# Kernel optimization log

Measured on AMD Instinct MI355X. Metric: run time of the kernel, lower is better.

The kernel has to match this reference:

```python
import jax, jax.numpy as jnp
import numpy as np
import math

B, T, E, H = 2, 2048, 1024, 16
D = E // H  # head_dim = 64


def setup_inputs() -> dict:
    key = jax.random.key(0)
    ks = jax.random.split(key, 8)
    s = 1.0 / math.sqrt(E)
    x = jax.random.normal(ks[0], (B, T, E), dtype=jnp.float32)
    # Linear weights stored as [in, out] so y = x @ W (equivalent to torch x @ W.T)
    Wq = jax.random.normal(ks[1], (E, E), dtype=jnp.float32) * s
    Wk = jax.random.normal(ks[2], (E, E), dtype=jnp.float32) * s
    Wv = jax.random.normal(ks[3], (E, E), dtype=jnp.float32) * s
    Wa = jax.random.normal(ks[4], (E, H), dtype=jnp.float32) * s
    Wg = jax.random.normal(ks[5], (E, E), dtype=jnp.float32) * s
    Wo = jax.random.normal(ks[6], (E, E), dtype=jnp.float32) * s
    A_log = jnp.linspace(0.0, math.log(16.0), H, dtype=jnp.float32)
    dt_bias = jnp.zeros((H,), dtype=jnp.float32)
    rms_w = jnp.ones((D,), dtype=jnp.float32)
    return {"x": x, "Wq": Wq, "Wk": Wk, "Wv": Wv, "Wa": Wa, "Wg": Wg,
            "Wo": Wo, "A_log": A_log, "dt_bias": dt_bias, "rms_w": rms_w}


def _l2norm(t):
    n = jnp.linalg.norm(t, axis=-1, keepdims=True)
    return t / jnp.maximum(n, 1e-12)


def reference(x, Wq, Wk, Wv, Wa, Wg, Wo, A_log, dt_bias, rms_w):
    b, seq_len, e = x.shape
    h = A_log.shape[0]
    d = e // h
    # QKV projections, L2-normalize q and k over head_dim -> [b, h, t, d]
    q = _l2norm((x @ Wq).reshape(b, seq_len, h, d)).transpose(0, 2, 1, 3)
    k = _l2norm((x @ Wk).reshape(b, seq_len, h, d)).transpose(0, 2, 1, 3)
    v = (x @ Wv).reshape(b, seq_len, h, d).transpose(0, 2, 1, 3)
    # scalar decay alpha in (0,1]: exp(-exp(A_log) * softplus(x @ Wa + dt_bias))
    dt = jax.nn.softplus(x @ Wa + dt_bias)           # [b, t, h]
    alpha = jnp.exp(-jnp.exp(A_log) * dt)            # [b, t, h]
    # decay mask L_ij = prod_{s=j+1}^{i} alpha_s (i >= j), via cumulative log-sum
    cum_log = jnp.cumsum(jnp.log(alpha + 1e-8), axis=1).transpose(0, 2, 1)  # [b, h, t]
    log_l = cum_log[..., :, None] - cum_log[..., None, :]                   # [b, h, t, t]
    causal = jnp.tril(jnp.ones((seq_len, seq_len), dtype=bool))
    l_mat = jnp.where(causal, jnp.exp(log_l), 0.0)
    # quadratic form: Y = (L * Q K^T) V
    scores = jnp.einsum('bhid,bhjd->bhij', q, k) * l_mat
    out = jnp.einsum('bhij,bhjd->bhid', scores, v)   # [b, h, t, d]
    # RMSNorm over head_dim (eps=1e-6)
    out = out * jax.lax.rsqrt(jnp.mean(out * out, axis=-1, keepdims=True) + 1e-6) * rms_w
    out = out.transpose(0, 2, 1, 3).reshape(b, seq_len, e)
    gate = jax.nn.silu(x @ Wg)
    return (out * gate) @ Wo
```

## Files before the change

kernel.cpp:

```cpp
#include <hip/hip_runtime.h>
#include <hip/hip_bf16.h>
#include <math.h>

#define B_ 2
#define T_ 2048
#define E_ 1024
#define H_ 16
#define D_ 64
#define MTOK (B_*T_)

typedef __bf16 bf16;
typedef __bf16 bf16x8 __attribute__((ext_vector_type(8)));
typedef __bf16 bf16x4 __attribute__((ext_vector_type(4)));
typedef float  f32x4  __attribute__((ext_vector_type(4)));

__device__ __forceinline__ void gl_lds16(const void* g, void* l) {
    __builtin_amdgcn_global_load_lds(
        (const __attribute__((address_space(1))) void*)g,
        (__attribute__((address_space(3))) void*)l, 16, 0, 0);
}

__global__ __launch_bounds__(256) void prep_weights_kernel(
    const float* __restrict__ Wq, const float* __restrict__ Wk,
    const float* __restrict__ Wv, const float* __restrict__ Wg,
    const float* __restrict__ Wo, const float* __restrict__ Wa,
    bf16* __restrict__ WTqh, bf16* __restrict__ WTql,
    bf16* __restrict__ WTvg, bf16* __restrict__ WTo,
    float* __restrict__ WaT) {
    const int tid = threadIdx.x;
    if (blockIdx.x >= 1280) {
        int idx = (blockIdx.x - 1280) * 256 + tid;
        WaT[idx] = Wa[(idx & 1023)*H_ + (idx >> 10)];
        return;
    }
    __shared__ float ts[64][65];
    const int seg = blockIdx.x >> 8;
    const int bid = blockIdx.x & 255;
    const float* src = (seg == 0) ? Wq : (seg == 1) ? Wk : (seg == 2) ? Wv
                     : (seg == 3) ? Wg : Wo;
    const int bx = bid & 15, by = bid >> 4;
    {
        const int r = tid >> 2, cb = (tid & 3) * 16;
        const float* s = src + (size_t)(by*64 + r)*1024 + bx*64 + cb;
#pragma unroll
        for (int j = 0; j < 4; ++j) {
            float4 v = *(const float4*)(s + j*4);
            ts[r][cb + j*4 + 0] = v.x; ts[r][cb + j*4 + 1] = v.y;
            ts[r][cb + j*4 + 2] = v.z; ts[r][cb + j*4 + 3] = v.w;
        }
    }
    __syncthreads();
    const int c = tid >> 2, rb = (tid & 3) * 16;
    const size_t obase = (size_t)(bx*64 + c)*1024 + by*64 + rb;
    if (seg < 2) {
        bf16* dh = ((seg == 0) ? WTqh : WTqh + (size_t)1024*1024);
        bf16* dl = ((seg == 0) ? WTql : WTql + (size_t)1024*1024);
#pragma unroll
        for (int half = 0; half < 2; ++half) {
            bf16x8 hv, lv;
#pragma unroll
            for (int e = 0; e < 8; ++e) {
                float v = ts[rb + half*8 + e][c];
                bf16 h = (bf16)v;
                hv[e] = h;
                lv[e] = (bf16)(v - (float)h);
            }
            *(bf16x8*)(dh + obase + half*8) = hv;
            *(bf16x8*)(dl + obase + half*8) = lv;
        }
    } else {
        bf16* dst = (seg == 2) ? WTvg : (seg == 3) ? (WTvg + (size_t)1024*1024) : WTo;
#pragma unroll
        for (int half = 0; half < 2; ++half) {
            bf16x8 hv;
#pragma unroll
            for (int e = 0; e < 8; ++e)
                hv[e] = (bf16)ts[rb + half*8 + e][c];
            *(bf16x8*)(dst + obase + half*8) = hv;
        }
    }
}

__global__ __launch_bounds__(256) void dtx_kernel(const float* __restrict__ x,
                                                  const float* __restrict__ WaT,
                                                  const float* __restrict__ A_log,
                                                  const float* __restrict__ dt_bias,
                                                  float* __restrict__ lg,
                                                  bf16* __restrict__ xh,
                                                  bf16* __restrict__ xl) {
    __shared__ float xs[16][1032];
    const int tb = blockIdx.x * 16;
    const int tid = threadIdx.x;
#pragma unroll
    for (int v = tid; v < 2048; v += 256) {
        int row = v >> 7, c8 = (v & 127) * 8;
        const float* src = x + (size_t)(tb + row)*E_ + c8;
        float4 a = *(const float4*)src;
        float4 b = *(const float4*)(src + 4);
        float va[8] = {a.x, a.y, a.z, a.w, b.x, b.y, b.z, b.w};
        bf16x8 hv, lv;
#pragma unroll
        for (int j = 0; j < 8; ++j) {
            xs[row][c8+j] = va[j];
            bf16 h = (bf16)va[j];
            hv[j] = h;
            lv[j] = (bf16)(va[j] - (float)h);
        }
        *(bf16x8*)(xh + (size_t)(tb + row)*E_ + c8) = hv;
        *(bf16x8*)(xl + (size_t)(tb + row)*E_ + c8) = lv;
    }
    __syncthreads();
    const int i = tid >> 4, h = tid & 15;
    const float* wrow = WaT + (size_t)h*1024;
    float acc = 0.f;
#pragma unroll 8
    for (int k = 0; k < 1024; k += 4) {
        float4 xv = *(const float4*)&xs[i][k];
        float4 wv = *(const float4*)(wrow + k);
        acc += xv.x*wv.x + xv.y*wv.y + xv.z*wv.z + xv.w*wv.w;
    }
    float z   = acc + dt_bias[h];
    float dtv = (z > 20.f) ? z : log1pf(expf(z));
    float la  = -expf(A_log[h]) * dtv;
    float l   = logf(expf(la) + 1e-8f);
    int n = tb + i;
    int b = n / T_, t = n % T_;
    lg[(size_t)(b*H_ + h)*T_ + t] = l;
}

__global__ __launch_bounds__(256) void scan_kernel(const float* __restrict__ lg,
                                                   double* __restrict__ cl) {
    int row = blockIdx.x, tid = threadIdx.x;
    __shared__ double ls[256];
    const float* p = lg + (size_t)row*T_ + tid*8;
    double loc[8], s = 0.0;
#pragma unroll
    for (int j = 0; j < 8; ++j) { s += (double)p[j]; loc[j] = s; }
    ls[tid] = s;
    __syncthreads();
    for (int off = 1; off < 256; off <<= 1) {
        double add = (tid >= off) ? ls[tid - off] : 0.0;
        __syncthreads();
        ls[tid] += add;
        __syncthreads();
    }
    double prefix = ls[tid] - s;
    double* o = cl + (size_t)row*T_ + tid*8;
#pragma unroll
    for (int j = 0; j < 8; ++j) o[j] = prefix + loc[j];
}

__global__ __launch_bounds__(256, 2) void gemm_qkvg_kernel(
    const bf16* __restrict__ Ah, const bf16* __restrict__ Al,
    const bf16* __restrict__ Bh, const bf16* __restrict__ Bl,
    const bf16* __restrict__ BTvg,
    bf16* __restrict__ qhb, bf16* __restrict__ qlb,
    bf16* __restrict__ khb, bf16* __restrict__ klb,
    bf16* __restrict__ vt, float* __restrict__ Gf) {
    const int K = E_;
    __shared__ __align__(16) bf16 S[5][128*32];
    const int tid = threadIdx.x, lane = tid & 63, wid = tid >> 6;
    const int wr = wid >> 1, wc = wid & 1;
    const int lr = lane & 15, lg4 = lane >> 4;
    const int tr = tid >> 2;
    const int tc = ((tid & 3) ^ ((tid >> 3) & 3)) * 8;
    const int co = (lg4 ^ ((lr >> 1) & 3)) * 8;
    int bid = blockIdx.x;
    bid = (bid & 7) * 64 + (bid >> 3);
    const int bx = bid & 15, by = bid >> 4;
    f32x4 accq[4][4], accv[4][4];
#pragma unroll
    for (int m = 0; m < 4; ++m)
#pragma unroll
        for (int n = 0; n < 4; ++n) { accq[m][n] = (f32x4)0.0f; accv[m][n] = (f32x4)0.0f; }
    for (int k0 = 0; k0 < K; k0 += 32) {
#pragma unroll
        for (int i = 0; i < 2; ++i) {
            size_t ga = (size_t)(by*128 + i*64 + tr)*K + k0 + tc;
            size_t gb = (size_t)(bx*128 + i*64 + tr)*K + k0 + tc;
            gl_lds16(Ah   + ga, &S[0][(i*256 + wid*64)*8]);
            gl_lds16(Al   + ga, &S[1][(i*256 + wid*64)*8]);
            gl_lds16(Bh   + gb, &S[2][(i*256 + wid*64)*8]);
            gl_lds16(Bl   + gb, &S[3][(i*256 + wid*64)*8]);
            gl_lds16(BTvg + gb, &S[4][(i*256 + wid*64)*8]);
        }
        __syncthreads();
        bf16x8 ah[4], al[4], bh[4], bl[4], bv[4];
#pragma unroll
        for (int m = 0; m < 4; ++m) {
            int o = (wr*64 + m*16 + lr)*32 + co;
            ah[m] = *(const bf16x8*)&S[0][o];
            al[m] = *(const bf16x8*)&S[1][o];
        }
#pragma unroll
        for (int n = 0; n < 4; ++n) {
            int o = (wc*64 + n*16 + lr)*32 + co;
            bh[n] = *(const bf16x8*)&S[2][o];
            bl[n] = *(const bf16x8*)&S[3][o];
            bv[n] = *(const bf16x8*)&S[4][o];
        }
#pragma unroll
        for (int m = 0; m < 4; ++m)
#pragma unroll
            for (int n = 0; n < 4; ++n) {
                accq[m][n] = __builtin_amdgcn_mfma_f32_16x16x32_bf16(al[m], bh[n], accq[m][n], 0, 0, 0);
                accq[m][n] = __builtin_amdgcn_mfma_f32_16x16x32_bf16(ah[m], bl[n], accq[m][n], 0, 0, 0);
                accq[m][n] = __builtin_amdgcn_mfma_f32_16x16x32_bf16(ah[m], bh[n], accq[m][n], 0, 0, 0);
                accv[m][n] = __builtin_amdgcn_mfma_f32_16x16x32_bf16(ah[m], bv[n], accv[m][n], 0, 0, 0);
            }
        __syncthreads();
    }
    {
        const int headg = bx*2 + wc;
        bf16* dh = (headg < 16) ? qhb : khb;
        bf16* dl = (headg < 16) ? qlb : klb;
        const int h = headg & 15;
#pragma unroll
        for (int m = 0; m < 4; ++m)
#pragma unroll
            for (int r = 0; r < 4; ++r) {
                float ss = accq[m][0][r]*accq[m][0][r] + accq[m][1][r]*accq[m][1][r]
                         + accq[m][2][r]*accq[m][2][r] + accq[m][3][r]*accq[m][3][r];
#pragma unroll
                for (int off = 1; off < 16; off <<= 1) ss += __shfl_xor(ss, off, 64);
                float sc = 1.0f / fmaxf(sqrtf(ss), 1e-12f);
                int token = by*128 + wr*64 + m*16 + lg4*4 + r;
#pragma unroll
                for (int n = 0; n < 4; ++n) {
                    int d = n*16 + lr;
                    float qv = accq[m][n][r] * sc;
                    bf16 hv = (bf16)qv;
                    size_t idx = ((size_t)token*H_ + h)*64 + d;
                    dh[idx] = hv;
                    dl[idx] = (bf16)(qv - (float)hv);
                }
            }
    }
    {
        const int colbase = bx*128 + wc*64;
        const int b = by >> 4;
        if (colbase < 1024) {
            const int head = colbase >> 6;
#pragma unroll
            for (int m = 0; m < 4; ++m) {
                int trow = by*128 + wr*64 + m*16 + lg4*4;
                int tloc = trow - b*T_;
#pragma unroll
                for (int n = 0; n < 4; ++n) {
                    int d = n*16 + lr;
                    bf16x4 pk;
                    pk[0] = (bf16)accv[m][n][0]; pk[1] = (bf16)accv[m][n][1];
                    pk[2] = (bf16)accv[m][n][2]; pk[3] = (bf16)accv[m][n][3];
                    *(bf16x4*)(vt + ((size_t)((b*H_ + head)*64 + d))*T_ + tloc) = pk;
                }
            }
        } else {
#pragma unroll
            for (int m = 0; m < 4; ++m)
#pragma unroll
                for (int r = 0; r < 4; ++r) {
                    int token = by*128 + wr*64 + m*16 + lg4*4 + r;
#pragma unroll
                    for (int n = 0; n < 4; ++n) {
                        int colg = colbase - 1024 + n*16 + lr;
                        float g = accv[m][n][r];
                        Gf[(size_t)token*E_ + colg] = g / (1.0f + __expf(-g));
                    }
                }
        }
    }
}

__global__ __launch_bounds__(256) void gemm_out_kernel(
    const bf16* __restrict__ A, const bf16* __restrict__ BT, float* __restrict__ C) {
    const int K = E_, N = E_;
    __shared__ __align__(16) bf16 As[128*32];
    __shared__ __align__(16) bf16 Bs[64*32];
    int bid = blockIdx.x;
    bid = (bid & 7) * 64 + (bid >> 3);
    const int bx = bid & 15, by = bid >> 4;
    const int tid = threadIdx.x, lane = tid & 63, wid = tid >> 6;
    const int wr = wid >> 1, wc = wid & 1;
    const int lr = lane & 15, lg4 = lane >> 4;
    f32x4 acc[4][2];
#pragma unroll
    for (int m = 0; m < 4; ++m)
#pragma unroll
        for (int n = 0; n < 2; ++n) acc[m][n] = (f32x4)0.0f;
    const int tr = tid >> 2;
    const int tc = ((tid & 3) ^ ((tid >> 3) & 3)) * 8;
    const int co = (lg4 ^ ((lr >> 1) & 3)) * 8;
    for (int k0 = 0; k0 < K; k0 += 32) {
#pragma unroll
        for (int i = 0; i < 2; ++i)
            gl_lds16(A + (size_t)(by*128 + i*64 + tr)*K + k0 + tc, &As[(i*256 + wid*64)*8]);
        gl_lds16(BT + (size_t)(bx*64 + tr)*K + k0 + tc, &Bs[(wid*64)*8]);
        __syncthreads();
        bf16x8 af[4], bfr[2];
#pragma unroll
        for (int m = 0; m < 4; ++m)
            af[m] = *(const bf16x8*)&As[(wr*64 + m*16 + lr)*32 + co];
#pragma unroll
        for (int n = 0; n < 2; ++n)
            bfr[n] = *(const bf16x8*)&Bs[(wc*32 + n*16 + lr)*32 + co];
#pragma unroll
        for (int m = 0; m < 4; ++m)
#pragma unroll
            for (int n = 0; n < 2; ++n)
                acc[m][n] = __builtin_amdgcn_mfma_f32_16x16x32_bf16(af[m], bfr[n], acc[m][n], 0, 0, 0);
        __syncthreads();
    }
    const int crow = by*128 + wr*64;
    const int ccol = bx*64 + wc*32 + lr;
#pragma unroll
    for (int m = 0; m < 4; ++m)
#pragma unroll
        for (int r = 0; r < 4; ++r) {
            int row = crow + m*16 + lg4*4 + r;
#pragma unroll
            for (int n = 0; n < 2; ++n)
                C[(size_t)row*N + ccol + n*16] = acc[m][n][r];
        }
}

__global__ __launch_bounds__(256) void attn_kernel(
    const bf16* __restrict__ qh, const bf16* __restrict__ ql,
    const bf16* __restrict__ kh, const bf16* __restrict__ kl,
    const bf16* __restrict__ vt, const double* __restrict__ cl,
    const float* __restrict__ Gf, const float* __restrict__ rms_w,
    bf16* __restrict__ Y) {
    __shared__ __align__(16) bf16 Ksh[2][64*64];
    __shared__ __align__(16) bf16 Ksl[2][64*64];
    __shared__ __align__(16) bf16 Vs[2][64*64];
    __shared__ __align__(16) bf16 Ps[128*64];
    const int rank = blockIdx.x >> 5, bh = blockIdx.x & 31;
    const int it = (rank < 8) ? (15 - rank) : (rank - 8);
    const int b = bh >> 4, h = bh & 15;
    const int tid = threadIdx.x, lane = tid & 63, wid = tid >> 6;
    const int i0 = it * 128;
    const int lr = lane & 15, lg4 = lane >> 4;
    bf16x8 qfh[2][2], qfl[2][2];
#pragma unroll
    for (int mm = 0; mm < 2; ++mm) {
        int qtok = i0 + wid*32 + mm*16 + lr;
        size_t qa = (size_t)(b*T_ + qtok)*E_ + h*64 + lg4*8;
        qfh[mm][0] = *(const bf16x8*)(qh + qa);
        qfh[mm][1] = *(const bf16x8*)(qh + qa + 32);
        qfl[mm][0] = *(const bf16x8*)(ql + qa);
        qfl[mm][1] = *(const bf16x8*)(ql + qa + 32);
    }
    const double* clrow = cl + (size_t)bh*T_;
    const double base = clrow[i0];
    float cli2[2][4];
#pragma unroll
    for (int mm = 0; mm < 2; ++mm)
#pragma unroll
        for (int r = 0; r < 4; ++r)
            cli2[mm][r] = (float)(clrow[i0 + wid*32 + mm*16 + lg4*4 + r] - base);
    f32x4 oacc[2][4];
#pragma unroll
    for (int mm = 0; mm < 2; ++mm)
#pragma unroll
        for (int n = 0; n < 4; ++n) oacc[mm][n] = (f32x4)0.0f;
    const int srow8 = lane >> 3;
    const int csrc  = (lane & 7) ^ srow8;
    auto STAGE = [&](int jt, int buf) {
        const int j0 = jt * 64;
#pragma unroll
        for (int i = 0; i < 2; ++i) {
            int krow = j0 + i*32 + wid*8 + srow8;
            int drow = i*32 + wid*8 + srow8;
            size_t gk = (size_t)(b*T_ + krow)*E_ + h*64 + csrc*8;
            gl_lds16(kh + gk, &Ksh[buf][(i*32 + wid*8)*64]);
            gl_lds16(kl + gk, &Ksl[buf][(i*32 + wid*8)*64]);
            gl_lds16(vt + (size_t)(bh*64 + drow)*T_ + j0 + csrc*8, &Vs[buf][(i*32 + wid*8)*64]);
        }
    };
    const int niter = 2*it + 2;
    int jt_min;
    {
        int lo = 0, hi = niter - 1;
        while (lo < hi) {
            int mid = (lo + hi) >> 1;
            int jend = mid*64 + 63; if (jend > i0) jend = i0;
            if (clrow[jend] <= base + 95.0) hi = mid; else lo = mid + 1;
        }
        jt_min = lo;
    }
    STAGE(jt_min, 0);
    __syncthreads();
    int cur = 0;
    for (int jt = jt_min; jt < niter; ++jt) {
        const int j0 = jt * 64;
        if (jt + 1 < niter) STAGE(jt + 1, cur ^ 1);
#pragma unroll
        for (int n = 0; n < 4; ++n) {
            const int r = n*16 + lr;
            const int sw = r & 7;
            const int ko = r*64;
            bf16x8 k_h0 = *(const bf16x8*)&Ksh[cur][ko + ((lg4 ^ sw)*8)];
            bf16x8 k_h1 = *(const bf16x8*)&Ksh[cur][ko + (((lg4+4) ^ sw)*8)];
            bf16x8 k_l0 = *(const bf16x8*)&Ksl[cur][ko + ((lg4 ^ sw)*8)];
            bf16x8 k_l1 = *(const bf16x8*)&Ksl[cur][ko + (((lg4+4) ^ sw)*8)];
            const int j = j0 + r;
            const float cj = (float)(clrow[j] - base);
#pragma unroll
            for (int mm = 0; mm < 2; ++mm) {
                f32x4 s = (f32x4)0.0f;
                __builtin_amdgcn_s_setprio(1);
                s = __builtin_amdgcn_mfma_f32_16x16x32_bf16(qfl[mm][0], k_h0, s, 0, 0, 0);
                s = __builtin_amdgcn_mfma_f32_16x16x32_bf16(qfl[mm][1], k_h1, s, 0, 0, 0);
                s = __builtin_amdgcn_mfma_f32_16x16x32_bf16(qfh[mm][0], k_l0, s, 0, 0, 0);
                s = __builtin_amdgcn_mfma_f32_16x16x32_bf16(qfh[mm][1], k_l1, s, 0, 0, 0);
                s = __builtin_amdgcn_mfma_f32_16x16x32_bf16(qfh[mm][0], k_h0, s, 0, 0, 0);
                s = __builtin_amdgcn_mfma_f32_16x16x32_bf16(qfh[mm][1], k_h1, s, 0, 0, 0);
                __builtin_amdgcn_s_setprio(0);
                const int prbase = wid*32 + mm*16 + lg4*4;
#pragma unroll
                for (int r4 = 0; r4 < 4; ++r4) {
                    const int pr = prbase + r4;
                    const int qrow = i0 + pr;
                    float val = (j <= qrow)
                        ? s[r4] * __expf(cli2[mm][r4] - cj) : 0.0f;
                    const int cw = n*2 + (lr >> 3);
                    Ps[pr*64 + ((cw ^ (pr & 7))*8) + (lane & 7)] = (bf16)val;
                }
            }
        }
#pragma unroll
        for (int kk = 0; kk < 2; ++kk) {
            const int js = kk*4 + lg4;
            bf16x8 pf[2];
#pragma unroll
            for (int mm = 0; mm < 2; ++mm) {
                const int rp = wid*32 + mm*16 + lr;
                pf[mm] = *(const bf16x8*)&Ps[rp*64 + ((js ^ (rp & 7))*8)];
            }
            __builtin_amdgcn_s_setprio(1);
#pragma unroll
            for (int n = 0; n < 4; ++n) {
                const int rv = n*16 + lr;
                bf16x8 vf = *(const bf16x8*)&Vs[cur][rv*64 + ((js ^ (rv & 7))*8)];
                oacc[0][n] = __builtin_amdgcn_mfma_f32_16x16x32_bf16(pf[0], vf, oacc[0][n], 0, 0, 0);
                oacc[1][n] = __builtin_amdgcn_mfma_f32_16x16x32_bf16(pf[1], vf, oacc[1][n], 0, 0, 0);
            }
            __builtin_amdgcn_s_setprio(0);
        }
        __syncthreads();
        cur ^= 1;
    }
#pragma unroll
    for (int mm = 0; mm < 2; ++mm)
#pragma unroll
        for (int r = 0; r < 4; ++r) {
            float ss = oacc[mm][0][r]*oacc[mm][0][r] + oacc[mm][1][r]*oacc[mm][1][r]
                     + oacc[mm][2][r]*oacc[mm][2][r] + oacc[mm][3][r]*oacc[mm][3][r];
#pragma unroll
            for (int off = 1; off < 16; off <<= 1) ss += __shfl_xor(ss, off, 64);
            const float scale = rsqrtf(ss * (1.0f/64.0f) + 1e-6f);
            const int gtok = b*T_ + i0 + wid*32 + mm*16 + lg4*4 + r;
#pragma unroll
            for (int n = 0; n < 4; ++n) {
                const int d = n*16 + lr;
                float o = oacc[mm][n][r] * scale * rms_w[d];
                float gate = Gf[(size_t)gtok*E_ + h*64 + d];
                Y[(size_t)gtok*E_ + h*64 + d] = (bf16)(o * gate);
            }
        }
}

extern "C" void kernel_launch(void* const* d_in, const int* in_sizes, int n_in,
                              void* d_out, int out_size, void* d_ws, size_t ws_size,
                              hipStream_t stream) {
    const float* x       = (const float*)d_in[0];
    const float* Wq      = (const float*)d_in[1];
    const float* Wk      = (const float*)d_in[2];
    const float* Wv      = (const float*)d_in[3];
    const float* Wa      = (const float*)d_in[4];
    const float* Wg      = (const float*)d_in[5];
    const float* Wo      = (const float*)d_in[6];
    const float* A_log   = (const float*)d_in[7];
    const float* dt_bias = (const float*)d_in[8];
    const float* rms_w   = (const float*)d_in[9];
    float* out = (float*)d_out;

    char* w = (char*)d_ws;
    size_t off = 0;
    auto alloc = [&](size_t bytes) {
        void* p = w + off; off += (bytes + 255) & ~(size_t)255; return p;
    };
    bf16*   xh   = (bf16*)  alloc((size_t)MTOK*E_*2);
    bf16*   xl   = (bf16*)  alloc((size_t)MTOK*E_*2);
    bf16*   WTqh = (bf16*)  alloc((size_t)2048*E_*2);
    bf16*   WTql = (bf16*)  alloc((size_t)2048*E_*2);
    bf16*   WTvg = (bf16*)  alloc((size_t)2048*E_*2);
    bf16*   WTo  = (bf16*)  alloc((size_t)E_*E_*2);
    bf16*   qhb  = (bf16*)  alloc((size_t)MTOK*E_*2);
    bf16*   qlb  = (bf16*)  alloc((size_t)MTOK*E_*2);
    bf16*   khb  = (bf16*)  alloc((size_t)MTOK*E_*2);
    bf16*   klb  = (bf16*)  alloc((size_t)MTOK*E_*2);
    bf16*   vt   = (bf16*)  alloc((size_t)MTOK*E_*2);
    float*  Gf   = (float*) alloc((size_t)MTOK*E_*4);
    float*  lg   = (float*) alloc((size_t)B_*H_*T_*4);
    double* cl   = (double*)alloc((size_t)B_*H_*T_*8);
    bf16*   Yb   = (bf16*)  alloc((size_t)MTOK*E_*2);
    float*  WaT  = (float*) alloc((size_t)H_*E_*4);

    hipLaunchKernelGGL(prep_weights_kernel, dim3(1344), dim3(256), 0, stream,
                       Wq, Wk, Wv, Wg, Wo, Wa, WTqh, WTql, WTvg, WTo, WaT);

    hipLaunchKernelGGL(dtx_kernel, dim3(256), dim3(256), 0, stream,
                       x, WaT, A_log, dt_bias, lg, xh, xl);
    hipLaunchKernelGGL(scan_kernel, dim3(B_*H_), dim3(256), 0, stream, lg, cl);

    hipLaunchKernelGGL(gemm_qkvg_kernel, dim3(512), dim3(256), 0, stream,
                       xh, xl, WTqh, WTql, WTvg, qhb, qlb, khb, klb, vt, Gf);

    hipLaunchKernelGGL(attn_kernel, dim3(512), dim3(256), 0, stream,
                       qhb, qlb, khb, klb, vt, cl, Gf, rms_w, Yb);

    hipLaunchKernelGGL(gemm_out_kernel, dim3(512), dim3(256), 0, stream, Yb, WTo, out);
}
```

Baseline: 158.3 us.

## Fold scan into QKVG GEMM launch and widen output GEMM K-tile to 64

The separate prefix-scan kernel is removed, and its work now runs in 32 extra blocks appended to the QKVG GEMM grid, reusing that kernel's shared memory. This drops one kernel launch and lets the scan run alongside the GEMM blocks. Separately, the output GEMM now stages 64-wide K tiles with an XOR swizzle and issues two MFMAs per fragment pair, which halves the loop iterations and barriers. The cost is more LDS per block in the output GEMM, which could reduce occupancy.

```diff
diff --git a/kernel.cpp b/kernel.cpp
--- a/kernel.cpp
+++ b/kernel.cpp
@@ -128,38 +128,38 @@
     lg[(size_t)(b*H_ + h)*T_ + t] = l;
 }
 
-__global__ __launch_bounds__(256) void scan_kernel(const float* __restrict__ lg,
-                                                   double* __restrict__ cl) {
-    int row = blockIdx.x, tid = threadIdx.x;
-    __shared__ double ls[256];
-    const float* p = lg + (size_t)row*T_ + tid*8;
-    double loc[8], s = 0.0;
-#pragma unroll
-    for (int j = 0; j < 8; ++j) { s += (double)p[j]; loc[j] = s; }
-    ls[tid] = s;
-    __syncthreads();
-    for (int off = 1; off < 256; off <<= 1) {
-        double add = (tid >= off) ? ls[tid - off] : 0.0;
-        __syncthreads();
-        ls[tid] += add;
-        __syncthreads();
-    }
-    double prefix = ls[tid] - s;
-    double* o = cl + (size_t)row*T_ + tid*8;
-#pragma unroll
-    for (int j = 0; j < 8; ++j) o[j] = prefix + loc[j];
-}
-
 __global__ __launch_bounds__(256, 2) void gemm_qkvg_kernel(
     const bf16* __restrict__ Ah, const bf16* __restrict__ Al,
     const bf16* __restrict__ Bh, const bf16* __restrict__ Bl,
     const bf16* __restrict__ BTvg,
     bf16* __restrict__ qhb, bf16* __restrict__ qlb,
     bf16* __restrict__ khb, bf16* __restrict__ klb,
-    bf16* __restrict__ vt, float* __restrict__ Gf) {
+    bf16* __restrict__ vt, float* __restrict__ Gf,
+    const float* __restrict__ lg, double* __restrict__ cl) {
     const int K = E_;
     __shared__ __align__(16) bf16 S[5][128*32];
     const int tid = threadIdx.x, lane = tid & 63, wid = tid >> 6;
+    if (blockIdx.x >= 512) {
+        double* ls = (double*)&S[0][0];
+        int row = blockIdx.x - 512;
+        const float* p = lg + (size_t)row*T_ + tid*8;
+        double loc[8], s = 0.0;
+#pragma unroll
+        for (int j = 0; j < 8; ++j) { s += (double)p[j]; loc[j] = s; }
+        ls[tid] = s;
+        __syncthreads();
+        for (int off = 1; off < 256; off <<= 1) {
+            double add = (tid >= off) ? ls[tid - off] : 0.0;
+            __syncthreads();
+            ls[tid] += add;
+            __syncthreads();
+        }
+        double prefix = ls[tid] - s;
+        double* o = cl + (size_t)row*T_ + tid*8;
+#pragma unroll
+        for (int j = 0; j < 8; ++j) o[j] = prefix + loc[j];
+        return;
+    }
     const int wr = wid >> 1, wc = wid & 1;
     const int lr = lane & 15, lg4 = lane >> 4;
     const int tr = tid >> 2;
@@ -274,8 +274,8 @@
 __global__ __launch_bounds__(256) void gemm_out_kernel(
     const bf16* __restrict__ A, const bf16* __restrict__ BT, float* __restrict__ C) {
     const int K = E_, N = E_;
-    __shared__ __align__(16) bf16 As[128*32];
-    __shared__ __align__(16) bf16 Bs[64*32];
+    __shared__ __align__(16) bf16 As[128*64];
+    __shared__ __align__(16) bf16 Bs[64*64];
     int bid = blockIdx.x;
     bid = (bid & 7) * 64 + (bid >> 3);
     const int bx = bid & 15, by = bid >> 4;
@@ -287,27 +287,40 @@
     for (int m = 0; m < 4; ++m)
 #pragma unroll
         for (int n = 0; n < 2; ++n) acc[m][n] = (f32x4)0.0f;
-    const int tr = tid >> 2;
-    const int tc = ((tid & 3) ^ ((tid >> 3) & 3)) * 8;
-    const int co = (lg4 ^ ((lr >> 1) & 3)) * 8;
-    for (int k0 = 0; k0 < K; k0 += 32) {
-#pragma unroll
-        for (int i = 0; i < 2; ++i)
-            gl_lds16(A + (size_t)(by*128 + i*64 + tr)*K + k0 + tc, &As[(i*256 + wid*64)*8]);
-        gl_lds16(BT + (size_t)(bx*64 + tr)*K + k0 + tc, &Bs[(wid*64)*8]);
+    const int srow = lane >> 3;
+    const int csrc = ((lane & 7) ^ srow) * 8;
+    for (int k0 = 0; k0 < K; k0 += 64) {
+#pragma unroll
+        for (int i = 0; i < 4; ++i)
+            gl_lds16(A + (size_t)(by*128 + i*32 + wid*8 + srow)*K + k0 + csrc,
+                     &As[(i*32 + wid*8)*64]);
+#pragma unroll
+        for (int j = 0; j < 2; ++j)
+            gl_lds16(BT + (size_t)(bx*64 + j*32 + wid*8 + srow)*K + k0 + csrc,
+                     &Bs[(j*32 + wid*8)*64]);
         __syncthreads();
-        bf16x8 af[4], bfr[2];
+        bf16x8 af[4][2], bfr[2][2];
+#pragma unroll
+        for (int m = 0; m < 4; ++m) {
+            int row = wr*64 + m*16 + lr;
+#pragma unroll
+            for (int kk = 0; kk < 2; ++kk)
+                af[m][kk] = *(const bf16x8*)&As[row*64 + (((kk*4 + lg4) ^ (lr & 7))*8)];
+        }
+#pragma unroll
+        for (int n = 0; n < 2; ++n) {
+            int row = wc*32 + n*16 + lr;
+#pragma unroll
+            for (int kk = 0; kk < 2; ++kk)
+                bfr[n][kk] = *(const bf16x8*)&Bs[row*64 + (((kk*4 + lg4) ^ (lr & 7))*8)];
+        }
 #pragma unroll
         for (int m = 0; m < 4; ++m)
-            af[m] = *(const bf16x8*)&As[(wr*64 + m*16 + lr)*32 + co];
-#pragma unroll
-        for (int n = 0; n < 2; ++n)
-            bfr[n] = *(const bf16x8*)&Bs[(wc*32 + n*16 + lr)*32 + co];
-#pragma unroll
-        for (int m = 0; m < 4; ++m)
-#pragma unroll
-            for (int n = 0; n < 2; ++n)
-                acc[m][n] = __builtin_amdgcn_mfma_f32_16x16x32_bf16(af[m], bfr[n], acc[m][n], 0, 0, 0);
+#pragma unroll
+            for (int n = 0; n < 2; ++n) {
+                acc[m][n] = __builtin_amdgcn_mfma_f32_16x16x32_bf16(af[m][0], bfr[n][0], acc[m][n], 0, 0, 0);
+                acc[m][n] = __builtin_amdgcn_mfma_f32_16x16x32_bf16(af[m][1], bfr[n][1], acc[m][n], 0, 0, 0);
+            }
         __syncthreads();
     }
     const int crow = by*128 + wr*64;
@@ -511,10 +524,9 @@
 
     hipLaunchKernelGGL(dtx_kernel, dim3(256), dim3(256), 0, stream,
                        x, WaT, A_log, dt_bias, lg, xh, xl);
-    hipLaunchKernelGGL(scan_kernel, dim3(B_*H_), dim3(256), 0, stream, lg, cl);
-
-    hipLaunchKernelGGL(gemm_qkvg_kernel, dim3(512), dim3(256), 0, stream,
-                       xh, xl, WTqh, WTql, WTvg, qhb, qlb, khb, klb, vt, Gf);
+
+    hipLaunchKernelGGL(gemm_qkvg_kernel, dim3(544), dim3(256), 0, stream,
+                       xh, xl, WTqh, WTql, WTvg, qhb, qlb, khb, klb, vt, Gf, lg, cl);
 
     hipLaunchKernelGGL(attn_kernel, dim3(512), dim3(256), 0, stream,
                        qhb, qlb, khb, klb, vt, cl, Gf, rms_w, Yb);
```

Result: faster. 152.3 us (-3.8%).
